# Kernel tuning notes

Hardware: AMD Instinct MI355X
Metric: run time of the kernel (lower is better)

Reference implementation:

```python
import jax, jax.numpy as jnp
import numpy as np

B, T, D, H = 4, 2048, 1024, 16


def setup_inputs() -> dict:
    key = jax.random.key(0)
    ks = jax.random.split(key, 5)
    s = 0.02  # keep activations sane
    return {
        "x": jax.random.normal(ks[0], (B, T, D), jnp.float32),
        "Wq": jax.random.normal(ks[1], (D, D), jnp.float32) * s,
        "bq": jnp.zeros((D,), jnp.float32),
        "Wk": jax.random.normal(ks[2], (D, D), jnp.float32) * s,
        "bk": jnp.zeros((D,), jnp.float32),
        "Wv": jax.random.normal(ks[3], (D, D), jnp.float32) * s,
        "bv": jnp.zeros((D,), jnp.float32),
        "Wo": jax.random.normal(ks[4], (D, D), jnp.float32) * s,
        "bo": jnp.zeros((D,), jnp.float32),
    }


def _split_heads(t):  # (B,T,D) -> (B,H,T,d)
    b, s, d = t.shape
    return t.reshape(b, s, H, d // H).transpose(0, 2, 1, 3)


def reference(x, Wq, bq, Wk, bk, Wv, bv, Wo, bo):
    d_k = D // H
    q = _split_heads(x @ Wq + bq)  # (B,H,T,d)
    k = _split_heads(x @ Wk + bk)
    v = _split_heads(x @ Wv + bv)
    # scaled dot-product similarities (B,H,T,T)
    scores = jnp.einsum("bhqd,bhkd->bhqk", q, k) / jnp.sqrt(jnp.asarray(d_k, x.dtype))
    # causal mask: masked_fill(tril==0, -inf)
    causal = jnp.tril(jnp.ones((T, T), bool))
    scores = jnp.where(causal, scores, -jnp.inf)
    attn = jax.nn.softmax(scores, axis=-1)
    ctx = jnp.einsum("bhqk,bhkd->bhqd", attn, v)  # (B,H,T,d)
    ctx = ctx.transpose(0, 2, 1, 3).reshape(x.shape[0], T, D)
    return ctx @ Wo + bo
```

## Files before the change

kernel.cpp:

```cpp
#include <hip/hip_runtime.h>
#include <hip/hip_bf16.h>

typedef unsigned short u16;
typedef __attribute__((ext_vector_type(8))) short bf16x8;
typedef __attribute__((ext_vector_type(4))) short bf16x4;
typedef __attribute__((ext_vector_type(4))) float f32x4;

#define DD 1024
#define TT 2048
#define HH 16
#define BB 4
#define DK 64
#define MM 8192

#define QSCALE 0.180336880f

__device__ __forceinline__ u16 f2b(float x) {
  __hip_bfloat16 h = __float2bfloat16(x);
  return *reinterpret_cast<u16*>(&h);
}

__device__ __forceinline__ unsigned pk2(float a, float b) {
  float2 t; t.x = a; t.y = b;
  __hip_bfloat162 h = __float22bfloat162_rn(t);
  union { __hip_bfloat162 h; unsigned u; } cv;
  cv.h = h;
  return cv.u;
}

#define GLD16(gp, lp)                                                         \
  __builtin_amdgcn_global_load_lds(                                           \
      (const __attribute__((address_space(1))) unsigned int*)(gp),            \
      (__attribute__((address_space(3))) unsigned int*)(lp), 16, 0, 0)

__global__ __launch_bounds__(256) void cast_bf16_kernel(
    const float* __restrict__ src, u16* __restrict__ dst, int n) {
  int i = (blockIdx.x * 256 + threadIdx.x) * 4;
  if (i + 3 < n) {
    float4 v = *reinterpret_cast<const float4*>(src + i);
    ushort4 o;
    o.x = f2b(v.x); o.y = f2b(v.y); o.z = f2b(v.z); o.w = f2b(v.w);
    *reinterpret_cast<ushort4*>(dst + i) = o;
  }
}

__global__ __launch_bounds__(256) void transpose_cast_kernel(
    const float* __restrict__ W0, const float* __restrict__ W1,
    const float* __restrict__ W2, const float* __restrict__ W3,
    u16* __restrict__ O0, u16* __restrict__ O1,
    u16* __restrict__ O2, u16* __restrict__ O3) {
  const float* W; u16* O;
  switch (blockIdx.z) {
    case 0: W = W0; O = O0; break;
    case 1: W = W1; O = O1; break;
    case 2: W = W2; O = O2; break;
    default: W = W3; O = O3; break;
  }
  __shared__ float tile[32][33];
  int tx = threadIdx.x, ty = threadIdx.y;
  int bx = blockIdx.x * 32;
  int by = blockIdx.y * 32;
#pragma unroll
  for (int j = 0; j < 4; j++)
    tile[ty + j * 8][tx] = W[(size_t)(by + ty + j * 8) * DD + bx + tx];
  __syncthreads();
#pragma unroll
  for (int j = 0; j < 4; j++)
    O[(size_t)(bx + ty + j * 8) * DD + by + tx] = f2b(tile[tx][ty + j * 8]);
}

#define GEMM_STAGE(Aptr, Bptr, Asl, Bsl)                                      \
  _Pragma("unroll") for (int c = 0; c < 4; c++) {                             \
    int idx = tid * 8 + c * 2048;                                             \
    int row = idx >> 6, ck = idx & 63;                                        \
    int src = ck ^ ((row & 7) << 3);                                          \
    GLD16(Aptr + (size_t)(m0 + row) * DD + k0 + src, Asl + idx);              \
    GLD16(Bptr + (size_t)(n0 + row) * DD + k0 + src, Bsl + idx);              \
  }

#define GEMM_MFMA(Asl, Bsl)                                                   \
  _Pragma("unroll") for (int half = 0; half < 2; half++) {                    \
    bf16x8 af[4], bfr[4];                                                     \
    _Pragma("unroll") for (int mb = 0; mb < 4; mb++) {                        \
      int r = wm + mb * 16 + l16;                                             \
      af[mb] = *reinterpret_cast<const bf16x8*>(                              \
          &Asl[r * 64 + ((half * 32 + quad * 8) ^ ((r & 7) << 3))]);          \
    }                                                                         \
    _Pragma("unroll") for (int nb = 0; nb < 4; nb++) {                        \
      int r = wn + nb * 16 + l16;                                             \
      bfr[nb] = *reinterpret_cast<const bf16x8*>(                             \
          &Bsl[r * 64 + ((half * 32 + quad * 8) ^ ((r & 7) << 3))]);          \
    }                                                                         \
    _Pragma("unroll") for (int mb = 0; mb < 4; mb++)                          \
      _Pragma("unroll") for (int nb = 0; nb < 4; nb++)                        \
          acc[mb][nb] = __builtin_amdgcn_mfma_f32_16x16x32_bf16(              \
              af[mb], bfr[nb], acc[mb][nb], 0, 0, 0);                         \
  }

__global__ __launch_bounds__(256, 4) void gemm_qkv_kernel(
    const u16* __restrict__ A,
    const u16* __restrict__ WtQ, const u16* __restrict__ WtK,
    const u16* __restrict__ WtV,
    const float* __restrict__ bq, const float* __restrict__ bk,
    const float* __restrict__ bv,
    u16* __restrict__ Qo, u16* __restrict__ Ko, u16* __restrict__ Vo) {
  __shared__ __align__(16) u16 smem[17408];
  u16* As = smem;
  u16* Bs = smem + 8192;
  u16* Vs = smem;
  int z = blockIdx.z;
  const u16* Bt = (z == 0) ? WtQ : ((z == 1) ? WtK : WtV);
  const float* bias = (z == 0) ? bq : ((z == 1) ? bk : bv);
  int tid = threadIdx.x;
  int wave = tid >> 6, lane = tid & 63;
  int quad = lane >> 4, l16 = lane & 15;
  int m0 = blockIdx.x * 128, n0 = blockIdx.y * 128;
  int wm = (wave >> 1) * 64, wn = (wave & 1) * 64;

  f32x4 acc[4][4];
#pragma unroll
  for (int i = 0; i < 4; i++)
#pragma unroll
    for (int j = 0; j < 4; j++) acc[i][j] = (f32x4){0.f, 0.f, 0.f, 0.f};

  for (int k0 = 0; k0 < DD; k0 += 64) {
    GEMM_STAGE(A, Bt, As, Bs)
    __syncthreads();
    GEMM_MFMA(As, Bs)
    __syncthreads();
  }

  if (z == 2) {
#pragma unroll
    for (int mb = 0; mb < 4; mb++)
#pragma unroll
      for (int nb = 0; nb < 4; nb++) {
        int col = wn + nb * 16 + l16;
        float bv2 = bias[n0 + col];
#pragma unroll
        for (int r = 0; r < 4; r++) {
          int row = wm + mb * 16 + quad * 4 + r;
          Vs[col * 136 + row] = f2b(acc[mb][nb][r] + bv2);
        }
      }
    __syncthreads();
    int b = m0 >> 11;
    int tloc = m0 & 2047;
#pragma unroll
    for (int i = 0; i < 8; i++) {
      int idx = tid * 8 + i * 2048;
      int row = idx >> 7, col = idx & 127;
      uint4 v = *reinterpret_cast<const uint4*>(&Vs[row * 136 + col]);
      int ncol = n0 + row, h = ncol >> 6, dd = ncol & 63;
      *reinterpret_cast<uint4*>(
          Vo + (((size_t)(b * HH + h) * DK) + dd) * TT + tloc + col) = v;
    }
    return;
  }

  u16* outp = (z == 0) ? Qo : Ko;
  float scale = (z == 0) ? QSCALE : 1.0f;
#pragma unroll
  for (int mb = 0; mb < 4; mb++) {
#pragma unroll
    for (int nb = 0; nb < 4; nb++) {
      int col = n0 + wn + nb * 16 + l16;
      float bv2 = bias[col];
#pragma unroll
      for (int r = 0; r < 4; r++) {
        int row = m0 + wm + mb * 16 + quad * 4 + r;
        float val = (acc[mb][nb][r] + bv2) * scale;
        int hh = col >> 6, dd = col & 63;
        int b = row >> 11, t = row & 2047;
        outp[(((size_t)(b * HH + hh) * TT) + t) * DK + dd] = f2b(val);
      }
    }
  }
}

__global__ __launch_bounds__(256, 4) void gemm_out_kernel(
    const u16* __restrict__ A, const u16* __restrict__ Bt,
    const float* __restrict__ bias, float* __restrict__ outp) {
  __shared__ __align__(16) u16 As[128 * 64];
  __shared__ __align__(16) u16 Bs[128 * 64];
  int tid = threadIdx.x;
  int wave = tid >> 6, lane = tid & 63;
  int quad = lane >> 4, l16 = lane & 15;
  int m0 = blockIdx.x * 128, n0 = blockIdx.y * 128;
  int wm = (wave >> 1) * 64, wn = (wave & 1) * 64;

  f32x4 acc[4][4];
#pragma unroll
  for (int i = 0; i < 4; i++)
#pragma unroll
    for (int j = 0; j < 4; j++) acc[i][j] = (f32x4){0.f, 0.f, 0.f, 0.f};

  for (int k0 = 0; k0 < DD; k0 += 64) {
    GEMM_STAGE(A, Bt, As, Bs)
    __syncthreads();
    GEMM_MFMA(As, Bs)
    __syncthreads();
  }

#pragma unroll
  for (int mb = 0; mb < 4; mb++) {
#pragma unroll
    for (int nb = 0; nb < 4; nb++) {
      int col = n0 + wn + nb * 16 + l16;
      float bv = bias[col];
#pragma unroll
      for (int r = 0; r < 4; r++) {
        int row = m0 + wm + mb * 16 + quad * 4 + r;
        outp[(size_t)row * DD + col] = acc[mb][nb][r] + bv;
      }
    }
  }
}

__global__ __launch_bounds__(256, 2) void attn_kernel(
    const u16* __restrict__ Q, const u16* __restrict__ K,
    const u16* __restrict__ VT, u16* __restrict__ ctx) {
  __shared__ __align__(16) u16 Ks[2][128][64];
  __shared__ __align__(16) u16 Vt[2][64][128];

  int tid = threadIdx.x;
  int wave = tid >> 6, lane = tid & 63;
  int quad = lane >> 4, l16 = lane & 15;
  int bid = blockIdx.x;
  int bh = bid & 63;
  int px = bid >> 6;
  int b = bh >> 4, h = bh & 15;
  const u16* Qh = Q + (size_t)bh * TT * DK;
  const u16* Kh = K + (size_t)bh * TT * DK;
  const u16* Vh = VT + (size_t)bh * DK * TT;

  const bf16x4 ones = (bf16x4){0x3F80, 0x3F80, 0x3F80, 0x3F80};
  int l8 = l16 & 7;
  int ksw = l8 << 3;

#define ATTN_STAGE(bb, ktile)                                                 \
  _Pragma("unroll") for (int c = 0; c < 4; c++) {                             \
    int idx = tid * 8 + c * 2048;                                             \
    int krow = idx >> 6, kcol = idx & 63;                                     \
    GLD16(Kh + (size_t)(ktile) * 8192 + krow * 64 +                           \
              (kcol ^ ((krow & 7) << 3)),                                     \
          &Ks[bb][0][0] + idx);                                               \
    int vd = idx >> 7, vg = (idx & 127) >> 3;                                 \
    GLD16(Vh + (size_t)vd * TT + (ktile) * 128 + ((vg ^ (vd & 7)) << 3),      \
          &Vt[bb][0][0] + idx);                                               \
  }

  for (int phase = 0; phase < 2; phase++) {
    int qtc = phase ? px : (15 - px);
    __syncthreads();

    bf16x8 qf[2][2];
#pragma unroll
    for (int s = 0; s < 2; s++) {
      const u16* qrow =
          Qh + (size_t)(qtc * 128 + wave * 32 + s * 16 + l16) * DK + quad * 8;
      qf[s][0] = *reinterpret_cast<const bf16x8*>(qrow);
      qf[s][1] = *reinterpret_cast<const bf16x8*>(qrow + 32);
    }

    ATTN_STAGE(0, 0)
    __syncthreads();

    f32x4 oacc[2][4];
    f32x4 lsum[2];
#pragma unroll
    for (int s = 0; s < 2; s++) {
      lsum[s] = (f32x4){0.f, 0.f, 0.f, 0.f};
#pragma unroll
      for (int dt = 0; dt < 4; dt++) oacc[s][dt] = (f32x4){0.f, 0.f, 0.f, 0.f};
    }

    for (int kt = 0; kt <= qtc; kt++) {
      int cur = kt & 1, nxt = cur ^ 1;
      bool more = kt < qtc;
      bool diag = kt == qtc;
      if (more) {
        ATTN_STAGE(nxt, kt + 1)
      }

      __builtin_amdgcn_s_setprio(1);
#pragma unroll
      for (int kb = 0; kb < 8; kb++) {
        if (diag && kb > 2 * wave + 1) continue;
        int krow = kb * 16 + l16;
        bf16x8 kf0 =
            *reinterpret_cast<const bf16x8*>(&Ks[cur][krow][(quad * 8) ^ ksw]);
        bf16x8 kf1 = *reinterpret_cast<const bf16x8*>(
            &Ks[cur][krow][(32 + quad * 8) ^ ksw]);
        bf16x4 vf[4];
        int vcol = (((kb * 2 + (quad >> 1)) ^ l8) << 3) + (quad & 1) * 4;
#pragma unroll
        for (int dt = 0; dt < 4; dt++)
          vf[dt] =
              *reinterpret_cast<const bf16x4*>(&Vt[cur][dt * 16 + l16][vcol]);
#pragma unroll
        for (int s = 0; s < 2; s++) {
          if (diag && kb > 2 * wave + s) continue;
          f32x4 sacc = (f32x4){0.f, 0.f, 0.f, 0.f};
          sacc = __builtin_amdgcn_mfma_f32_16x16x32_bf16(kf0, qf[s][0], sacc, 0, 0, 0);
          sacc = __builtin_amdgcn_mfma_f32_16x16x32_bf16(kf1, qf[s][1], sacc, 0, 0, 0);
          if (diag && kb == 2 * wave + s) {
#pragma unroll
            for (int r = 0; r < 4; r++)
              if (quad * 4 + r > l16) sacc[r] = -__builtin_inff();
          }
          float p0 = __builtin_amdgcn_exp2f(sacc[0]);
          float p1 = __builtin_amdgcn_exp2f(sacc[1]);
          float p2 = __builtin_amdgcn_exp2f(sacc[2]);
          float p3 = __builtin_amdgcn_exp2f(sacc[3]);
          union { unsigned u[2]; bf16x4 v; } pk;
          pk.u[0] = pk2(p0, p1);
          pk.u[1] = pk2(p2, p3);
          lsum[s] = __builtin_amdgcn_mfma_f32_16x16x16bf16_1k(pk.v, ones, lsum[s], 0, 0, 0);
#pragma unroll
          for (int dt = 0; dt < 4; dt++)
            oacc[s][dt] = __builtin_amdgcn_mfma_f32_16x16x16bf16_1k(
                pk.v, vf[dt], oacc[s][dt], 0, 0, 0);
        }
      }
      __builtin_amdgcn_s_setprio(0);

      __syncthreads();
    }

    f32x4 inv[2];
#pragma unroll
    for (int s = 0; s < 2; s++)
#pragma unroll
      for (int r = 0; r < 4; r++) inv[s][r] = 1.0f / lsum[s][r];

    u16* Obuf = &Ks[0][0][0];
#pragma unroll
    for (int s = 0; s < 2; s++)
#pragma unroll
      for (int dt = 0; dt < 4; dt++)
#pragma unroll
        for (int r = 0; r < 4; r++)
          Obuf[(wave * 32 + s * 16 + quad * 4 + r) * 64 + dt * 16 + l16] =
              f2b(oacc[s][dt][r] * inv[s][r]);
    asm volatile("s_waitcnt lgkmcnt(0)" ::: "memory");
#pragma unroll
    for (int i = 0; i < 4; i++) {
      int idx = lane * 8 + i * 512;
      int row = idx >> 6, colc = idx & 63;
      uint4 v =
          *reinterpret_cast<const uint4*>(&Obuf[(wave * 32 + row) * 64 + colc]);
      int t = qtc * 128 + wave * 32 + row;
      *reinterpret_cast<uint4*>(
          ctx + ((size_t)(b * TT + t)) * DD + h * DK + colc) = v;
    }
  }
#undef ATTN_STAGE
}

extern "C" void kernel_launch(void* const* d_in, const int* in_sizes, int n_in,
                              void* d_out, int out_size, void* d_ws, size_t ws_size,
                              hipStream_t stream) {
  const float* x  = (const float*)d_in[0];
  const float* Wq = (const float*)d_in[1];
  const float* bq = (const float*)d_in[2];
  const float* Wk = (const float*)d_in[3];
  const float* bk = (const float*)d_in[4];
  const float* Wv = (const float*)d_in[5];
  const float* bv = (const float*)d_in[6];
  const float* Wo = (const float*)d_in[7];
  const float* bo = (const float*)d_in[8];
  float* out = (float*)d_out;

  char* ws = (char*)d_ws;
  size_t off = 0;
  u16* xb  = (u16*)(ws + off); off += (size_t)MM * DD * 2;
  u16* wtq = (u16*)(ws + off); off += (size_t)DD * DD * 2;
  u16* wtk = (u16*)(ws + off); off += (size_t)DD * DD * 2;
  u16* wtv = (u16*)(ws + off); off += (size_t)DD * DD * 2;
  u16* wto = (u16*)(ws + off); off += (size_t)DD * DD * 2;
  u16* Qb  = (u16*)(ws + off); off += (size_t)MM * DD * 2;
  u16* Kb  = (u16*)(ws + off); off += (size_t)MM * DD * 2;
  u16* VTb = (u16*)(ws + off); off += (size_t)MM * DD * 2;
  u16* ctx = (u16*)(ws + off); off += (size_t)MM * DD * 2;

  {
    int n = MM * DD;
    cast_bf16_kernel<<<n / 1024, 256, 0, stream>>>(x, xb, n);
  }
  {
    dim3 grid(DD / 32, DD / 32, 4);
    dim3 block(32, 8);
    transpose_cast_kernel<<<grid, block, 0, stream>>>(Wq, Wk, Wv, Wo, wtq, wtk, wtv, wto);
  }
  {
    dim3 grid(MM / 128, DD / 128, 3);
    gemm_qkv_kernel<<<grid, 256, 0, stream>>>(xb, wtq, wtk, wtv, bq, bk, bv,
                                              Qb, Kb, VTb);
  }
  {
    attn_kernel<<<512, 256, 0, stream>>>(Qb, Kb, VTb, ctx);
  }
  {
    dim3 grid(MM / 128, DD / 128);
    gemm_out_kernel<<<grid, 256, 0, stream>>>(ctx, wto, bo, out);
  }
}
```

Measured before the change: 228.3 us.

## Use K=32 MFMA for P·V by pairing key blocks and buffering scores

Computes all QK^T score tiles for the 128-key block first and stores them in registers. It then pairs adjacent 16-key blocks so that P·V and the row-sum use the 16x16x32 bf16 MFMA instead of 16x16x16, which halves the number of PV MFMA issues. V fragments are built from two 4-element LDS reads per 8-element operand, and the causal mask is adjusted for the paired blocks. The cost is much higher register pressure from holding 16 score accumulators, which may reduce occupancy or cause spills, and the skip condition on the QK loop was removed on the diagonal tile.

```diff
diff --git a/kernel.cpp b/kernel.cpp
--- a/kernel.cpp
+++ b/kernel.cpp
@@ -234,7 +234,8 @@
   const u16* Kh = K + (size_t)bh * TT * DK;
   const u16* Vh = VT + (size_t)bh * DK * TT;
 
-  const bf16x4 ones = (bf16x4){0x3F80, 0x3F80, 0x3F80, 0x3F80};
+  const bf16x8 ones8 = (bf16x8){0x3F80, 0x3F80, 0x3F80, 0x3F80,
+                                0x3F80, 0x3F80, 0x3F80, 0x3F80};
   int l8 = l16 & 7;
   int ksw = l8 << 3;
 
@@ -284,6 +285,8 @@
       }
 
       __builtin_amdgcn_s_setprio(1);
+
+      f32x4 sacc[8][2];
 #pragma unroll
       for (int kb = 0; kb < 8; kb++) {
         if (diag && kb > 2 * wave + 1) continue;
@@ -292,35 +295,67 @@
             *reinterpret_cast<const bf16x8*>(&Ks[cur][krow][(quad * 8) ^ ksw]);
         bf16x8 kf1 = *reinterpret_cast<const bf16x8*>(
             &Ks[cur][krow][(32 + quad * 8) ^ ksw]);
-        bf16x4 vf[4];
-        int vcol = (((kb * 2 + (quad >> 1)) ^ l8) << 3) + (quad & 1) * 4;
-#pragma unroll
-        for (int dt = 0; dt < 4; dt++)
-          vf[dt] =
-              *reinterpret_cast<const bf16x4*>(&Vt[cur][dt * 16 + l16][vcol]);
 #pragma unroll
         for (int s = 0; s < 2; s++) {
-          if (diag && kb > 2 * wave + s) continue;
-          f32x4 sacc = (f32x4){0.f, 0.f, 0.f, 0.f};
-          sacc = __builtin_amdgcn_mfma_f32_16x16x32_bf16(kf0, qf[s][0], sacc, 0, 0, 0);
-          sacc = __builtin_amdgcn_mfma_f32_16x16x32_bf16(kf1, qf[s][1], sacc, 0, 0, 0);
-          if (diag && kb == 2 * wave + s) {
-#pragma unroll
-            for (int r = 0; r < 4; r++)
-              if (quad * 4 + r > l16) sacc[r] = -__builtin_inff();
+          f32x4 t = (f32x4){0.f, 0.f, 0.f, 0.f};
+          t = __builtin_amdgcn_mfma_f32_16x16x32_bf16(kf0, qf[s][0], t, 0, 0, 0);
+          t = __builtin_amdgcn_mfma_f32_16x16x32_bf16(kf1, qf[s][1], t, 0, 0, 0);
+          sacc[kb][s] = t;
+        }
+      }
+
+#pragma unroll
+      for (int j = 0; j < 4; j++) {
+        if (diag && j > wave) continue;
+        bf16x8 vf8[4];
+        int gl = ((j * 4 + (quad >> 1)) ^ l8) << 3;
+        int gh = ((j * 4 + 2 + (quad >> 1)) ^ l8) << 3;
+        int off = (quad & 1) * 4;
+#pragma unroll
+        for (int dt = 0; dt < 4; dt++) {
+          union { bf16x4 h[2]; bf16x8 v; } vv;
+          vv.h[0] = *reinterpret_cast<const bf16x4*>(
+              &Vt[cur][dt * 16 + l16][gl + off]);
+          vv.h[1] = *reinterpret_cast<const bf16x4*>(
+              &Vt[cur][dt * 16 + l16][gh + off]);
+          vf8[dt] = vv.v;
+        }
+#pragma unroll
+        for (int s = 0; s < 2; s++) {
+          f32x4 lo = sacc[2 * j][s];
+          f32x4 hi = sacc[2 * j + 1][s];
+          if (diag && j == wave) {
+            if (s == 0) {
+#pragma unroll
+              for (int r = 0; r < 4; r++) {
+                if (quad * 4 + r > l16) lo[r] = -__builtin_inff();
+                hi[r] = -__builtin_inff();
+              }
+            } else {
+#pragma unroll
+              for (int r = 0; r < 4; r++)
+                if (quad * 4 + r > l16) hi[r] = -__builtin_inff();
+            }
           }
-          float p0 = __builtin_amdgcn_exp2f(sacc[0]);
-          float p1 = __builtin_amdgcn_exp2f(sacc[1]);
-          float p2 = __builtin_amdgcn_exp2f(sacc[2]);
-          float p3 = __builtin_amdgcn_exp2f(sacc[3]);
-          union { unsigned u[2]; bf16x4 v; } pk;
+          float p0 = __builtin_amdgcn_exp2f(lo[0]);
+          float p1 = __builtin_amdgcn_exp2f(lo[1]);
+          float p2 = __builtin_amdgcn_exp2f(lo[2]);
+          float p3 = __builtin_amdgcn_exp2f(lo[3]);
+          float p4 = __builtin_amdgcn_exp2f(hi[0]);
+          float p5 = __builtin_amdgcn_exp2f(hi[1]);
+          float p6 = __builtin_amdgcn_exp2f(hi[2]);
+          float p7 = __builtin_amdgcn_exp2f(hi[3]);
+          union { unsigned u[4]; bf16x8 v; } pk;
           pk.u[0] = pk2(p0, p1);
           pk.u[1] = pk2(p2, p3);
-          lsum[s] = __builtin_amdgcn_mfma_f32_16x16x16bf16_1k(pk.v, ones, lsum[s], 0, 0, 0);
+          pk.u[2] = pk2(p4, p5);
+          pk.u[3] = pk2(p6, p7);
+          lsum[s] = __builtin_amdgcn_mfma_f32_16x16x32_bf16(
+              pk.v, ones8, lsum[s], 0, 0, 0);
 #pragma unroll
           for (int dt = 0; dt < 4; dt++)
-            oacc[s][dt] = __builtin_amdgcn_mfma_f32_16x16x16bf16_1k(
-                pk.v, vf[dt], oacc[s][dt], 0, 0, 0);
+            oacc[s][dt] = __builtin_amdgcn_mfma_f32_16x16x32_bf16(
+                pk.v, vf8[dt], oacc[s][dt], 0, 0, 0);
         }
       }
       __builtin_amdgcn_s_setprio(0);
```

New measurement: 224.3 us. No clear change (-1.7%).
